# Kernel optimization log

Hardware: AMD Instinct MI355X
Metric: run time of the kernel (lower is better)

Reference implementation:

```python
import jax, jax.numpy as jnp
import numpy as np

WIDTH = 2048
NUM_HEADS = 16
HEAD_DIM = WIDTH // NUM_HEADS
WINDOW = 1024
B, T = 4, 2048
MIN_LOGIT = -2.3819763e+38
MAX_WAVELENGTH = 10000.0


def apply_rope(x, positions):
    # x: [b, t, n, h]; RoPE on first half of h, pass-through second half
    b, t, n, h = x.shape
    x_rope, x_pass = jnp.split(x, 2, axis=-1)
    half = x_rope.shape[-1] // 2
    freq_exponents = 2.0 * jnp.arange(half, dtype=jnp.float32) / (2 * half)
    inv_freq = MAX_WAVELENGTH ** (-freq_exponents)  # [half]
    sinusoid = positions.astype(jnp.float32).reshape(1, t, 1, 1) * inv_freq  # [1,t,1,half]
    sin = jnp.sin(sinusoid).astype(x.dtype)
    cos = jnp.cos(sinusoid).astype(x.dtype)
    x1, x2 = jnp.split(x_rope, 2, axis=-1)
    return jnp.concatenate([x1 * cos - x2 * sin, x2 * cos + x1 * sin, x_pass], axis=-1)


def setup_inputs() -> dict:
    key = jax.random.key(0)
    ks = jax.random.split(key, 6)
    x = jax.random.normal(ks[0], (B, T, WIDTH), dtype=jnp.float32)
    segment_pos = jnp.arange(T, dtype=jnp.int32)
    # forward-pass mask: single segment, causal + window
    pos = jnp.arange(T)
    attention_mask = (pos[:, None] >= pos[None, :]) & (pos[:, None] <= pos[None, :] + WINDOW)
    std = np.sqrt(1.0 / WIDTH)
    wq = jax.random.normal(ks[1], (WIDTH, WIDTH), dtype=jnp.float32) * std
    wk = jax.random.normal(ks[2], (HEAD_DIM, WIDTH), dtype=jnp.float32) * std
    wv = jax.random.normal(ks[3], (HEAD_DIM, WIDTH), dtype=jnp.float32) * std
    w_out = jax.random.normal(ks[4], (WIDTH, WIDTH), dtype=jnp.float32) * std
    b_out = jnp.zeros((WIDTH,), dtype=jnp.float32)
    return {"x": x, "segment_pos": segment_pos, "attention_mask": attention_mask,
            "wq": wq, "wk": wk, "wv": wv, "w_out": w_out, "b_out": b_out}


def reference(x, segment_pos, attention_mask, wq, wk, wv, w_out, b_out):
    b, t, _ = x.shape
    q = (x @ wq.T).reshape(b, t, NUM_HEADS, HEAD_DIM)  # [b,t,n,h]
    k = (x @ wk.T).reshape(b, t, 1, HEAD_DIM)          # single shared KV head (MQA)
    v = x @ wv.T                                        # [b,t,h]
    q = apply_rope(q, segment_pos)
    k = apply_rope(k, segment_pos)[:, :, 0]             # [b,t,h]
    logits = jnp.einsum('btnh,bsh->bnts', q, k).astype(jnp.float32) * (HEAD_DIM ** -0.5)
    logits = jnp.where(attention_mask[None, None], logits, MIN_LOGIT)
    probs = jax.nn.softmax(logits, axis=-1).astype(x.dtype)
    encoded = jnp.einsum('bnts,bsh->btnh', probs, v).reshape(b, t, WIDTH)
    return encoded @ w_out.T + b_out
```

## Files before the change

kernel.cpp:

```cpp
#include <hip/hip_runtime.h>
#include <stdint.h>


#define WIDTH_ 2048
#define NHEADS_ 16
#define HD_ 128
#define WINDOW_ 1024
#define B_ 4
#define T_ 2048
#define MROWS_ (B_ * T_)
#define NQKV_ (WIDTH_ + 2 * HD_)

typedef float f32x4 __attribute__((ext_vector_type(4)));
typedef __bf16 bf16x8 __attribute__((ext_vector_type(8)));
typedef float f32x4v __attribute__((ext_vector_type(4)));
typedef unsigned short u16;
typedef unsigned int u32;

__device__ __forceinline__ u16 f2bf(float x) {
  u32 u = __builtin_bit_cast(u32, x);
  return (u16)((u + 0x7FFFu + ((u >> 16) & 1u)) >> 16);
}
__device__ __forceinline__ float bf2f(u16 b) {
  u32 u = ((u32)b) << 16;
  return __builtin_bit_cast(float, u);
}
__device__ __forceinline__ u32 pack2bf(float a, float b) {
  union { __bf16 h[2]; u32 u; } c;
  c.h[0] = (__bf16)a; c.h[1] = (__bf16)b;
  return c.u;
}

__device__ __forceinline__ f32x4 mfma16(bf16x8 a, bf16x8 b, f32x4 c) {
  return __builtin_amdgcn_mfma_f32_16x16x32_bf16(a, b, c, 0, 0, 0);
}

#define GLL16(gp, lp)                                          \
  __builtin_amdgcn_global_load_lds(                            \
      (const __attribute__((address_space(1))) void*)(gp),     \
      (__attribute__((address_space(3))) void*)(lp), 16, 0, 0)

#define CSC_ 0.12753101296631838f
#define L2C_ 0.4152410118609203f

__global__ __launch_bounds__(256) void cvt_all(const float* __restrict__ x,
                                               const float* __restrict__ wq,
                                               const float* __restrict__ wk,
                                               const float* __restrict__ wv,
                                               const float* __restrict__ wo,
                                               u16* __restrict__ xb,
                                               u16* __restrict__ wqkv,
                                               u16* __restrict__ wob) {
  const int NX = MROWS_ * WIDTH_ / 4;
  const int NQ = WIDTH_ * WIDTH_ / 4;
  const int NK = HD_ * WIDTH_ / 4;
  const int total = NX + 2 * NQ + 2 * NK;
  int i = blockIdx.x * blockDim.x + threadIdx.x;
  int stride = gridDim.x * blockDim.x;
  for (; i < total; i += stride) {
    const float* s;
    u16* d;
    int j;
    if (i < NX) { s = x; d = xb; j = i; }
    else if (i < NX + NQ) { s = wq; d = wqkv; j = i - NX; }
    else if (i < NX + NQ + NK) { s = wk; d = wqkv + (size_t)WIDTH_ * WIDTH_; j = i - NX - NQ; }
    else if (i < NX + NQ + 2 * NK) { s = wv; d = wqkv + (size_t)(WIDTH_ + HD_) * WIDTH_; j = i - NX - NQ - NK; }
    else { s = wo; d = wob; j = i - NX - NQ - 2 * NK; }
    f32x4v v = *reinterpret_cast<const f32x4v*>(s + 4 * (size_t)j);
    uint2 o;
    o.x = (u32)f2bf(v[0]) | ((u32)f2bf(v[1]) << 16);
    o.y = (u32)f2bf(v[2]) | ((u32)f2bf(v[3]) << 16);
    *reinterpret_cast<uint2*>(d + 4 * (size_t)j) = o;
  }
}

__global__ __launch_bounds__(256) void sincos_tab(const int* __restrict__ segpos,
                                                  float2* __restrict__ sc) {
  int idx = blockIdx.x * 256 + threadIdx.x;
  int t = idx >> 5, d = idx & 31;
  float pos = (float)segpos[t];
  float ang = pos * exp2f(-(float)d * L2C_);
  float2 v;
  v.x = cosf(ang);
  v.y = sinf(ang);
  sc[idx] = v;
}

template <bool F32OUT>
__global__ __launch_bounds__(256) void gemm_bt(const u16* __restrict__ A,
                                               const u16* __restrict__ W,
                                               void* __restrict__ Cout,
                                               const float* __restrict__ bias,
                                               int M, int N, int K) {
  __shared__ alignas(16) u16 As[128 * 32];
  __shared__ alignas(16) u16 Bs[128 * 32];
  const int tid = threadIdx.x;
  const int wid = tid >> 6, lane = tid & 63;
  const int g = lane >> 4, lr = lane & 15;
  const int m0 = blockIdx.y << 7, n0 = blockIdx.x << 7;
  const int wm = wid >> 1, wn = wid & 1;

  const f32x4 vzero = {0.f, 0.f, 0.f, 0.f};
  f32x4 acc[4][4];
#pragma unroll
  for (int i = 0; i < 4; i++)
#pragma unroll
    for (int j = 0; j < 4; j++) acc[i][j] = vzero;

  const int c0 = wid * 2, c1 = wid * 2 + 1;
  const int lrow = lane >> 2;
  const int lcol = (lane & 3) * 8;
  const u16* a0 = A + (size_t)(m0 + c0 * 16 + lrow) * K + lcol;
  const u16* a1 = A + (size_t)(m0 + c1 * 16 + lrow) * K + lcol;
  const u16* b0 = W + (size_t)(n0 + c0 * 16 + lrow) * K + lcol;
  const u16* b1 = W + (size_t)(n0 + c1 * 16 + lrow) * K + lcol;

  for (int k0 = 0; k0 < K; k0 += 32) {
    __syncthreads();
    GLL16(a0 + k0, &As[c0 * 512]);
    GLL16(a1 + k0, &As[c1 * 512]);
    GLL16(b0 + k0, &Bs[c0 * 512]);
    GLL16(b1 + k0, &Bs[c1 * 512]);
    __syncthreads();

    bf16x8 af[4], bfv[4];
#pragma unroll
    for (int mi = 0; mi < 4; mi++)
      af[mi] = *(const bf16x8*)&As[(wm * 64 + mi * 16 + lr) * 32 + g * 8];
#pragma unroll
    for (int ni = 0; ni < 4; ni++)
      bfv[ni] = *(const bf16x8*)&Bs[(wn * 64 + ni * 16 + lr) * 32 + g * 8];
#pragma unroll
    for (int mi = 0; mi < 4; mi++)
#pragma unroll
      for (int ni = 0; ni < 4; ni++)
        acc[mi][ni] = mfma16(af[mi], bfv[ni], acc[mi][ni]);
  }

#pragma unroll
  for (int mi = 0; mi < 4; mi++) {
    int row = m0 + wm * 64 + mi * 16 + g * 4;
#pragma unroll
    for (int ni = 0; ni < 4; ni++) {
      int col = n0 + wn * 64 + ni * 16 + lr;
#pragma unroll
      for (int r = 0; r < 4; r++) {
        float v = acc[mi][ni][r];
        if (F32OUT) {
          ((float*)Cout)[(size_t)(row + r) * N + col] = v + bias[col];
        } else {
          ((u16*)Cout)[(size_t)(row + r) * N + col] = f2bf(v);
        }
      }
    }
  }
}

template <bool F32OUT>
__global__ __launch_bounds__(512, 2) void gemm256p8(const u16* __restrict__ A,
                                                    const u16* __restrict__ W,
                                                    void* __restrict__ Cout,
                                                    const float* __restrict__ bias,
                                                    int M, int N, int K) {
  __shared__ alignas(16) u16 As[2][2][128 * 64];
  __shared__ alignas(16) u16 Bs[2][2][128 * 64];
  const int tid = threadIdx.x;
  const int wid = tid >> 6, lane = tid & 63;
  const int g = lane >> 4, lr = lane & 15;
  const int wm = wid >> 2, wn = wid & 3;

  const int nwg = gridDim.x;
  const int o = blockIdx.x;
  const int wg = (o & 7) * (nwg >> 3) + (o >> 3);
  const int NT = N >> 8;
  const int mt = wg / NT, nt = wg % NT;
  const int m0 = mt << 8, n0 = nt << 8;

  const u16* pa[2];
  const u16* pb[2];
#pragma unroll
  for (int j = 0; j < 2; j++) {
    int ci = (wid + j * 8) * 64 + lane;
    int ri = ci >> 3, c = ci & 7;
    int colel = (c ^ (ri & 7)) * 8;
    int rA = ((ri >> 6) << 7) + (ri & 63);
    pa[j] = A + (size_t)(m0 + rA) * K + colel;
    pb[j] = W + (size_t)(n0 + ri) * K + colel;
  }
  const int dstoff = wid * 1024;

#define SA(bi, h, k0)                                                     \
  do {                                                                    \
    GLL16(pa[0] + (size_t)(h) * 64 * K + (k0), (char*)As[bi][h] + dstoff);\
    GLL16(pa[1] + (size_t)(h) * 64 * K + (k0),                            \
          (char*)As[bi][h] + dstoff + 8192);                              \
  } while (0)
#define SB(bi, h, k0)                                                     \
  do {                                                                    \
    GLL16(pb[0] + (size_t)(h) * 128 * K + (k0), (char*)Bs[bi][h] + dstoff);\
    GLL16(pb[1] + (size_t)(h) * 128 * K + (k0),                           \
          (char*)Bs[bi][h] + dstoff + 8192);                              \
  } while (0)

  const f32x4 vzero = {0.f, 0.f, 0.f, 0.f};
  f32x4 acc[8][4];
#pragma unroll
  for (int i = 0; i < 8; i++)
#pragma unroll
    for (int j = 0; j < 4; j++) acc[i][j] = vzero;

  bf16x8 bfv[4][2];

  auto LDA = [&](int bi, int mi, int kk) -> bf16x8 {
    int h = mi >> 2;
    int rb = wm * 64 + (mi & 3) * 16 + lr;
    return *(const bf16x8*)((const char*)As[bi][h] + rb * 128 +
                            (((kk * 4 + g) ^ (lr & 7)) << 4));
  };
  auto LDB = [&](int bi, int ni, int kk) -> bf16x8 {
    int rb = (wn & 1) * 64 + ni * 16 + lr;
    return *(const bf16x8*)((const char*)Bs[bi][wn >> 1] + rb * 128 +
                            (((kk * 4 + g) ^ (lr & 7)) << 4));
  };

#define VM6 asm volatile("s_waitcnt vmcnt(6)" ::: "memory")
#define VM0 asm volatile("s_waitcnt vmcnt(0)" ::: "memory")

#define PHASE(bi, p, STAGES, VM)                                          \
  {                                                                       \
    if ((p) == 0) {                                                       \
      for (int ni = 0; ni < 4; ni++)                                      \
        for (int kk = 0; kk < 2; kk++) bfv[ni][kk] = LDB(bi, ni, kk);     \
    }                                                                     \
    bf16x8 a0k0 = LDA(bi, 2 * (p), 0);                                    \
    bf16x8 a0k1 = LDA(bi, 2 * (p), 1);                                    \
    bf16x8 a1k0 = LDA(bi, 2 * (p) + 1, 0);                                \
    bf16x8 a1k1 = LDA(bi, 2 * (p) + 1, 1);                                \
    STAGES;                                                               \
    __builtin_amdgcn_s_barrier();                                         \
    asm volatile("s_waitcnt lgkmcnt(0)" ::: "memory");                    \
    __builtin_amdgcn_sched_barrier(0);                                    \
    __builtin_amdgcn_s_setprio(1);                                        \
    for (int ni = 0; ni < 4; ni++) {                                      \
      acc[2 * (p)][ni] = mfma16(a0k0, bfv[ni][0], acc[2 * (p)][ni]);      \
      acc[2 * (p)][ni] = mfma16(a0k1, bfv[ni][1], acc[2 * (p)][ni]);      \
      acc[2 * (p) + 1][ni] = mfma16(a1k0, bfv[ni][0], acc[2 * (p) + 1][ni]); \
      acc[2 * (p) + 1][ni] = mfma16(a1k1, bfv[ni][1], acc[2 * (p) + 1][ni]); \
    }                                                                     \
    __builtin_amdgcn_s_setprio(0);                                        \
    VM;                                                                   \
    __builtin_amdgcn_sched_barrier(0);                                    \
    __builtin_amdgcn_s_barrier();                                         \
  }

  SA(0, 0, 0); SA(0, 1, 0); SB(0, 0, 0); SB(0, 1, 0);
  SB(1, 0, 64); SB(1, 1, 64); SA(1, 0, 64);
  VM6;
  __builtin_amdgcn_sched_barrier(0);
  __builtin_amdgcn_s_barrier();

  const int half_iters = K >> 7;
  for (int i = 0; i < half_iters; ++i) {
    const bool pre = (i + 1 < half_iters);
    const int kc = i << 7;
    PHASE(0, 0, { SA(1, 1, kc + 64); }, );
    PHASE(0, 1, { if (pre) SB(0, 0, kc + 128); }, );
    PHASE(0, 2, { if (pre) SB(0, 1, kc + 128); }, );
    PHASE(0, 3, { if (pre) SA(0, 0, kc + 128); }, if (pre) { VM6; } else { VM0; });
    PHASE(1, 0, { if (pre) SA(0, 1, kc + 128); }, );
    PHASE(1, 1, { if (pre) SB(1, 0, kc + 192); }, );
    PHASE(1, 2, { if (pre) SB(1, 1, kc + 192); }, );
    PHASE(1, 3, { if (pre) SA(1, 0, kc + 192); }, if (pre) { VM6; } else { VM0; });
  }
#undef PHASE
#undef SA
#undef SB
#undef VM6
#undef VM0

#pragma unroll
  for (int mi = 0; mi < 8; mi++) {
    int row = m0 + wm * 128 + mi * 16 + g * 4;
#pragma unroll
    for (int ni = 0; ni < 4; ni++) {
      int col = n0 + wn * 64 + ni * 16 + lr;
#pragma unroll
      for (int r = 0; r < 4; r++) {
        float v = acc[mi][ni][r];
        if (F32OUT) {
          ((float*)Cout)[(size_t)(row + r) * N + col] = v + bias[col];
        } else {
          ((u16*)Cout)[(size_t)(row + r) * N + col] = f2bf(v);
        }
      }
    }
  }
}

__global__ __launch_bounds__(128) void kv_scatter(const u16* __restrict__ KVraw,
                                                  const int* __restrict__ segpos,
                                                  u16* __restrict__ Kb,
                                                  u16* __restrict__ VT) {
  const int row = blockIdx.x;
  const int b = row / T_, t = row % T_;
  const float pos = (float)segpos[t];
  const u16* kvsrc = KVraw + (size_t)row * 256;
  const int tid = threadIdx.x;

  if (tid < 32) {
    int d = tid;
    float inv = exp2f(-(float)d * L2C_);
    float ang = pos * inv;
    float sn = sinf(ang), cs = cosf(ang);
    float x1 = bf2f(kvsrc[d]), x2 = bf2f(kvsrc[d + 32]);
    Kb[(size_t)row * HD_ + d] = f2bf(x1 * cs - x2 * sn);
    Kb[(size_t)row * HD_ + d + 32] = f2bf(x2 * cs + x1 * sn);
  } else if (tid >= 64 && tid < 128) {
    int d = tid;
    Kb[(size_t)row * HD_ + d] = kvsrc[d];
  }
  for (int j = tid; j < HD_; j += 128) {
    VT[((size_t)b * HD_ + j) * T_ + t] = kvsrc[HD_ + j];
  }
}

__global__ __launch_bounds__(512, 4) void attn(const u16* __restrict__ Qraw,
                                               const float2* __restrict__ sc,
                                               const u16* __restrict__ Kb,
                                               const u16* __restrict__ VT,
                                               u16* __restrict__ Eb) {
  __shared__ alignas(16) u16 Ks[2][64 * 128];
  __shared__ alignas(16) u16 Vs[2][128 * 64];
  __shared__ alignas(16) u16 Ps[8][16 * 64];

  const int tid = threadIdx.x;
  const int wid = tid >> 6, lane = tid & 63;
  const int g = lane >> 4, lr = lane & 15;

  const int bid = blockIdx.x;
  const int grp = bid >> 4;
  const int b = grp >> 4, n = grp & 15;
  const int qt = ((bid & 15) + b * 4) & 15;
  const int q0b = qt * 128;
  const int q0w = q0b + wid * 16;
  const int q = q0w + lr;

  const char* kptr = (const char*)(Kb + (size_t)b * T_ * HD_);
  const char* vptr = (const char*)(VT + (size_t)b * HD_ * T_);

  const char* srcb[4];
  int smul, dst0;
  if (wid < 4) {
    smul = HD_ * 2;
#pragma unroll
    for (int i = 0; i < 4; i++) {
      int row = wid * 16 + i * 4 + (lane >> 4);
      int c = (lane & 15) << 4;
      srcb[i] = kptr + (size_t)row * 256 + (c ^ ((row & 7) << 4));
    }
    dst0 = wid * 4096;
  } else {
    smul = 2;
#pragma unroll
    for (int i = 0; i < 4; i++) {
      int row = (wid - 4) * 32 + i * 8 + (lane >> 3);
      int c = (lane & 7) << 4;
      srcb[i] = vptr + (size_t)row * (T_ * 2) + (c ^ ((row & 7) << 4));
    }
    dst0 = (wid - 4) * 4096;
  }

  bf16x8 qf[4];
  {
    const float2* scp = sc + (size_t)q * 32 + g * 8;
    const u16* qp = Qraw + (size_t)(b * T_ + q) * WIDTH_ + n * HD_;
    bf16x8 r0 = *(const bf16x8*)(qp + g * 8);
    bf16x8 r1 = *(const bf16x8*)(qp + 32 + g * 8);
    bf16x8 r2 = *(const bf16x8*)(qp + 64 + g * 8);
    bf16x8 r3 = *(const bf16x8*)(qp + 96 + g * 8);
#pragma unroll
    for (int j = 0; j < 8; j++) {
      float2 cs2 = scp[j];
      float x1 = (float)r0[j], x2 = (float)r1[j];
      qf[0][j] = (__bf16)((x1 * cs2.x - x2 * cs2.y) * CSC_);
      qf[1][j] = (__bf16)((x2 * cs2.x + x1 * cs2.y) * CSC_);
      qf[2][j] = (__bf16)((float)r2[j] * CSC_);
      qf[3][j] = (__bf16)((float)r3[j] * CSC_);
    }
  }

  const f32x4 vzero = {0.f, 0.f, 0.f, 0.f};
  f32x4 eacc[8];
#pragma unroll
  for (int i = 0; i < 8; i++) eacc[i] = vzero;
  float m_r = -1e30f, l_r = 0.f;

  const int sbeg = (q0b > WINDOW_) ? (q0b - WINDOW_) : 0;
  const int nt = (q0b + 127 - sbeg) / 64 + 1;

  char* Pw = (char*)Ps[wid];
  const int swz = (lr & 7) << 4;

  auto STAGE = [&](int s0, int buf) {
    char* dbase = (wid < 4) ? ((char*)Ks[buf] + dst0) : ((char*)Vs[buf] + dst0);
#pragma unroll
    for (int i = 0; i < 4; i++) {
      GLL16(srcb[i] + (size_t)s0 * smul, dbase + i * 1024);
    }
  };

  STAGE(sbeg, 0);
  __syncthreads();

  for (int t = 0; t < nt; ++t) {
    const int s0 = sbeg + t * 64;
    const int cur = t & 1;
    if (t + 1 < nt) STAGE(s0 + 64, cur ^ 1);

    const bool active = (s0 <= q0w + 15) && (s0 + 63 >= q0w - WINDOW_);
    if (active) {
      const char* kB = (const char*)Ks[cur];
      const char* vB = (const char*)Vs[cur];
      f32x4 sacc[4];
#pragma unroll
      for (int h = 0; h < 4; h++) sacc[h] = vzero;
#pragma unroll
      for (int h = 0; h < 4; h++) {
        const int krow = h * 16 + lr;
#pragma unroll
        for (int kk = 0; kk < 4; kk++) {
          bf16x8 kf = *(const bf16x8*)(kB + krow * 256 + ((kk * 64 + g * 16) ^ swz));
          sacc[h] = mfma16(kf, qf[kk], sacc[h]);
        }
      }

      const bool wint = (s0 + 63 <= q0w) && (s0 >= q0w + 15 - WINDOW_);
      float pm = -1e30f;
      if (wint) {
#pragma unroll
        for (int h = 0; h < 4; h++)
#pragma unroll
          for (int r = 0; r < 4; r++) pm = fmaxf(pm, sacc[h][r]);
      } else {
#pragma unroll
        for (int h = 0; h < 4; h++)
#pragma unroll
          for (int r = 0; r < 4; r++) {
            int s = s0 + h * 16 + g * 4 + r;
            bool ok = (s <= q) && (s + WINDOW_ >= q);
            float v = ok ? sacc[h][r] : -1e30f;
            sacc[h][r] = v;
            pm = fmaxf(pm, v);
          }
      }
      pm = fmaxf(pm, __shfl_xor(pm, 16));
      pm = fmaxf(pm, __shfl_xor(pm, 32));

      if (!__all(pm <= m_r + 8.f)) {
        float mnew = fmaxf(m_r, pm);
        float alpha = exp2f(m_r - mnew);
        m_r = mnew;
        l_r *= alpha;
        float aq[4];
#pragma unroll
        for (int r = 0; r < 4; r++) aq[r] = __shfl(alpha, g * 4 + r);
#pragma unroll
        for (int i = 0; i < 8; i++) {
          f32x4 e = eacc[i];
#pragma unroll
          for (int r = 0; r < 4; r++) e[r] *= aq[r];
          eacc[i] = e;
        }
      }
      float rs = 0.f;
#pragma unroll
      for (int h = 0; h < 4; h++)
#pragma unroll
        for (int r = 0; r < 4; r++) {
          float e = exp2f(sacc[h][r] - m_r);
          sacc[h][r] = e;
          rs += e;
        }
      rs += __shfl_xor(rs, 16);
      rs += __shfl_xor(rs, 32);
      l_r += rs;

#pragma unroll
      for (int h = 0; h < 4; h++) {
        int base = (lr * 128 + h * 32 + g * 8) ^ swz;
        uint2 w2;
        w2.x = pack2bf(sacc[h][0], sacc[h][1]);
        w2.y = pack2bf(sacc[h][2], sacc[h][3]);
        *(uint2*)(Pw + base) = w2;
      }
      bf16x8 pf0 = *(const bf16x8*)(Pw + ((lr * 128 + g * 16) ^ swz));
      bf16x8 pf1 = *(const bf16x8*)(Pw + ((lr * 128 + 64 + g * 16) ^ swz));

#pragma unroll
      for (int ht = 0; ht < 8; ht++) {
        const int vrow = ht * 16 + lr;
        bf16x8 vf0 = *(const bf16x8*)(vB + vrow * 128 + ((g * 16) ^ swz));
        bf16x8 vf1 = *(const bf16x8*)(vB + vrow * 128 + ((64 + g * 16) ^ swz));
        eacc[ht] = mfma16(pf0, vf0, eacc[ht]);
        eacc[ht] = mfma16(pf1, vf1, eacc[ht]);
      }
    }
    __syncthreads();
  }

  float lq[4];
#pragma unroll
  for (int r = 0; r < 4; r++) lq[r] = 1.f / __shfl(l_r, g * 4 + r);
#pragma unroll
  for (int ht = 0; ht < 8; ht++) {
#pragma unroll
    for (int r = 0; r < 4; r++) {
      int row = b * T_ + q0w + g * 4 + r;
      int col = n * HD_ + ht * 16 + lr;
      Eb[(size_t)row * WIDTH_ + col] = f2bf(eacc[ht][r] * lq[r]);
    }
  }
}

extern "C" void kernel_launch(void* const* d_in, const int* in_sizes, int n_in,
                              void* d_out, int out_size, void* d_ws, size_t ws_size,
                              hipStream_t stream) {
  (void)in_sizes; (void)n_in; (void)out_size; (void)ws_size;
  const float* x = (const float*)d_in[0];
  const int* segpos = (const int*)d_in[1];
  const float* wq = (const float*)d_in[3];
  const float* wk = (const float*)d_in[4];
  const float* wv = (const float*)d_in[5];
  const float* w_out = (const float*)d_in[6];
  const float* b_out = (const float*)d_in[7];

  char* p = (char*)d_ws;
  u16* xb = (u16*)p;    p += (size_t)MROWS_ * WIDTH_ * 2;
  u16* wqkv = (u16*)p;  p += (size_t)NQKV_ * WIDTH_ * 2;
  u16* wob = (u16*)p;   p += (size_t)WIDTH_ * WIDTH_ * 2;
  u16* qraw = (u16*)p;  p += (size_t)MROWS_ * WIDTH_ * 2;
  u16* kvraw = (u16*)p; p += (size_t)MROWS_ * 256 * 2;
  u16* kb = (u16*)p;    p += (size_t)MROWS_ * HD_ * 2;
  u16* vt = (u16*)p;    p += (size_t)B_ * HD_ * T_ * 2;
  float2* sc = (float2*)p; p += (size_t)T_ * 32 * 8;
  u16* eb = xb;

  cvt_all<<<4096, 256, 0, stream>>>(x, wq, wk, wv, w_out, xb, wqkv, wob);
  sincos_tab<<<T_ * 32 / 256, 256, 0, stream>>>(segpos, sc);

  gemm256p8<false><<<(MROWS_ / 256) * (WIDTH_ / 256), 512, 0, stream>>>(
      xb, wqkv, qraw, nullptr, MROWS_, WIDTH_, WIDTH_);
  gemm_bt<false><<<dim3(256 / 128, MROWS_ / 128), 256, 0, stream>>>(
      xb, wqkv + (size_t)WIDTH_ * WIDTH_, kvraw, nullptr, MROWS_, 256, WIDTH_);

  kv_scatter<<<MROWS_, 128, 0, stream>>>(kvraw, segpos, kb, vt);
  attn<<<B_ * NHEADS_ * (T_ / 128), 512, 0, stream>>>(qraw, sc, kb, vt, eb);

  gemm256p8<true><<<(MROWS_ / 256) * (WIDTH_ / 256), 512, 0, stream>>>(
      eb, wob, d_out, b_out, MROWS_, WIDTH_, WIDTH_);
}
```

Measured before the change: 317.5 us.

## Rework attention to 32x32 MFMA tiles with register-shuffled P and narrower KV GEMM tiles

The attention kernel drops from 8 to 4 waves per block, and each wave now handles 32 query rows using 32x32x16 bf16 MFMAs. Probabilities are passed to the PV product through cross-lane shuffles, so the per-wave LDS P buffer and its write/read round trip are gone. The K/V staging layout and swizzle change to match the new fragment shapes. Separately, the small KV projection GEMM uses 64-wide N tiles, doubling its block count for better CU occupancy. In exchange, attention uses more accumulator registers per wave and fewer waves per block.

```diff
diff --git a/kernel.cpp b/kernel.cpp
--- a/kernel.cpp
+++ b/kernel.cpp
@@ -12,6 +12,7 @@
 #define NQKV_ (WIDTH_ + 2 * HD_)
 
 typedef float f32x4 __attribute__((ext_vector_type(4)));
+typedef float f32x16 __attribute__((ext_vector_type(16)));
 typedef __bf16 bf16x8 __attribute__((ext_vector_type(8)));
 typedef float f32x4v __attribute__((ext_vector_type(4)));
 typedef unsigned short u16;
@@ -33,6 +34,9 @@
 
 __device__ __forceinline__ f32x4 mfma16(bf16x8 a, bf16x8 b, f32x4 c) {
   return __builtin_amdgcn_mfma_f32_16x16x32_bf16(a, b, c, 0, 0, 0);
+}
+__device__ __forceinline__ f32x16 mfma32(bf16x8 a, bf16x8 b, f32x16 c) {
+  return __builtin_amdgcn_mfma_f32_32x32x16_bf16(a, b, c, 0, 0, 0);
 }
 
 #define GLL16(gp, lp)                                          \
@@ -86,54 +90,49 @@
   sc[idx] = v;
 }
 
-template <bool F32OUT>
-__global__ __launch_bounds__(256) void gemm_bt(const u16* __restrict__ A,
-                                               const u16* __restrict__ W,
-                                               void* __restrict__ Cout,
-                                               const float* __restrict__ bias,
-                                               int M, int N, int K) {
+__global__ __launch_bounds__(256) void gemm_bt64(const u16* __restrict__ A,
+                                                 const u16* __restrict__ W,
+                                                 u16* __restrict__ Cout,
+                                                 int M, int N, int K) {
   __shared__ alignas(16) u16 As[128 * 32];
-  __shared__ alignas(16) u16 Bs[128 * 32];
+  __shared__ alignas(16) u16 Bs[64 * 32];
   const int tid = threadIdx.x;
   const int wid = tid >> 6, lane = tid & 63;
   const int g = lane >> 4, lr = lane & 15;
-  const int m0 = blockIdx.y << 7, n0 = blockIdx.x << 7;
+  const int m0 = blockIdx.y << 7, n0 = blockIdx.x << 6;
   const int wm = wid >> 1, wn = wid & 1;
 
   const f32x4 vzero = {0.f, 0.f, 0.f, 0.f};
-  f32x4 acc[4][4];
+  f32x4 acc[4][2];
 #pragma unroll
   for (int i = 0; i < 4; i++)
 #pragma unroll
-    for (int j = 0; j < 4; j++) acc[i][j] = vzero;
-
-  const int c0 = wid * 2, c1 = wid * 2 + 1;
+    for (int j = 0; j < 2; j++) acc[i][j] = vzero;
+
   const int lrow = lane >> 2;
   const int lcol = (lane & 3) * 8;
-  const u16* a0 = A + (size_t)(m0 + c0 * 16 + lrow) * K + lcol;
-  const u16* a1 = A + (size_t)(m0 + c1 * 16 + lrow) * K + lcol;
-  const u16* b0 = W + (size_t)(n0 + c0 * 16 + lrow) * K + lcol;
-  const u16* b1 = W + (size_t)(n0 + c1 * 16 + lrow) * K + lcol;
+  const u16* a0 = A + (size_t)(m0 + wid * 32 + lrow) * K + lcol;
+  const u16* a1 = A + (size_t)(m0 + wid * 32 + 16 + lrow) * K + lcol;
+  const u16* b0 = W + (size_t)(n0 + wid * 16 + lrow) * K + lcol;
 
   for (int k0 = 0; k0 < K; k0 += 32) {
     __syncthreads();
-    GLL16(a0 + k0, &As[c0 * 512]);
-    GLL16(a1 + k0, &As[c1 * 512]);
-    GLL16(b0 + k0, &Bs[c0 * 512]);
-    GLL16(b1 + k0, &Bs[c1 * 512]);
+    GLL16(a0 + k0, &As[wid * 1024]);
+    GLL16(a1 + k0, &As[wid * 1024 + 512]);
+    GLL16(b0 + k0, &Bs[wid * 512]);
     __syncthreads();
 
-    bf16x8 af[4], bfv[4];
+    bf16x8 af[4], bfv[2];
 #pragma unroll
     for (int mi = 0; mi < 4; mi++)
       af[mi] = *(const bf16x8*)&As[(wm * 64 + mi * 16 + lr) * 32 + g * 8];
 #pragma unroll
-    for (int ni = 0; ni < 4; ni++)
-      bfv[ni] = *(const bf16x8*)&Bs[(wn * 64 + ni * 16 + lr) * 32 + g * 8];
+    for (int ni = 0; ni < 2; ni++)
+      bfv[ni] = *(const bf16x8*)&Bs[(wn * 32 + ni * 16 + lr) * 32 + g * 8];
 #pragma unroll
     for (int mi = 0; mi < 4; mi++)
 #pragma unroll
-      for (int ni = 0; ni < 4; ni++)
+      for (int ni = 0; ni < 2; ni++)
         acc[mi][ni] = mfma16(af[mi], bfv[ni], acc[mi][ni]);
   }
 
@@ -141,17 +140,11 @@
   for (int mi = 0; mi < 4; mi++) {
     int row = m0 + wm * 64 + mi * 16 + g * 4;
 #pragma unroll
-    for (int ni = 0; ni < 4; ni++) {
-      int col = n0 + wn * 64 + ni * 16 + lr;
-#pragma unroll
-      for (int r = 0; r < 4; r++) {
-        float v = acc[mi][ni][r];
-        if (F32OUT) {
-          ((float*)Cout)[(size_t)(row + r) * N + col] = v + bias[col];
-        } else {
-          ((u16*)Cout)[(size_t)(row + r) * N + col] = f2bf(v);
-        }
-      }
+    for (int ni = 0; ni < 2; ni++) {
+      int col = n0 + wn * 32 + ni * 16 + lr;
+#pragma unroll
+      for (int r = 0; r < 4; r++)
+        Cout[(size_t)(row + r) * N + col] = f2bf(acc[mi][ni][r]);
     }
   }
 }
@@ -324,87 +317,87 @@
   }
 }
 
-__global__ __launch_bounds__(512, 4) void attn(const u16* __restrict__ Qraw,
+__global__ __launch_bounds__(256, 2) void attn(const u16* __restrict__ Qraw,
                                                const float2* __restrict__ sc,
                                                const u16* __restrict__ Kb,
                                                const u16* __restrict__ VT,
                                                u16* __restrict__ Eb) {
   __shared__ alignas(16) u16 Ks[2][64 * 128];
   __shared__ alignas(16) u16 Vs[2][128 * 64];
-  __shared__ alignas(16) u16 Ps[8][16 * 64];
 
   const int tid = threadIdx.x;
   const int wid = tid >> 6, lane = tid & 63;
-  const int g = lane >> 4, lr = lane & 15;
+  const int qc = lane & 31, hi = lane >> 5;
 
   const int bid = blockIdx.x;
   const int grp = bid >> 4;
   const int b = grp >> 4, n = grp & 15;
   const int qt = ((bid & 15) + b * 4) & 15;
   const int q0b = qt * 128;
-  const int q0w = q0b + wid * 16;
-  const int q = q0w + lr;
+  const int q0w = q0b + wid * 32;
+  const int q = q0w + qc;
 
   const char* kptr = (const char*)(Kb + (size_t)b * T_ * HD_);
   const char* vptr = (const char*)(VT + (size_t)b * HD_ * T_);
 
-  const char* srcb[4];
+  const char* srcb[8];
   int smul, dst0;
-  if (wid < 4) {
+  if (wid < 2) {
     smul = HD_ * 2;
 #pragma unroll
-    for (int i = 0; i < 4; i++) {
-      int row = wid * 16 + i * 4 + (lane >> 4);
+    for (int i = 0; i < 8; i++) {
+      int row = wid * 32 + i * 4 + (lane >> 4);
       int c = (lane & 15) << 4;
-      srcb[i] = kptr + (size_t)row * 256 + (c ^ ((row & 7) << 4));
-    }
-    dst0 = wid * 4096;
+      srcb[i] = kptr + (size_t)row * 256 + (c ^ ((row & 15) << 4));
+    }
+    dst0 = wid * 8192;
   } else {
     smul = 2;
 #pragma unroll
-    for (int i = 0; i < 4; i++) {
-      int row = (wid - 4) * 32 + i * 8 + (lane >> 3);
+    for (int i = 0; i < 8; i++) {
+      int row = (wid - 2) * 64 + i * 8 + (lane >> 3);
       int c = (lane & 7) << 4;
       srcb[i] = vptr + (size_t)row * (T_ * 2) + (c ^ ((row & 7) << 4));
     }
-    dst0 = (wid - 4) * 4096;
-  }
-
-  bf16x8 qf[4];
+    dst0 = (wid - 2) * 8192;
+  }
+
+  bf16x8 qf[8];
   {
-    const float2* scp = sc + (size_t)q * 32 + g * 8;
-    const u16* qp = Qraw + (size_t)(b * T_ + q) * WIDTH_ + n * HD_;
-    bf16x8 r0 = *(const bf16x8*)(qp + g * 8);
-    bf16x8 r1 = *(const bf16x8*)(qp + 32 + g * 8);
-    bf16x8 r2 = *(const bf16x8*)(qp + 64 + g * 8);
-    bf16x8 r3 = *(const bf16x8*)(qp + 96 + g * 8);
+    const u16* qp = Qraw + (size_t)(b * T_ + q) * WIDTH_ + n * HD_ + hi * 8;
+    bf16x8 r[8];
+#pragma unroll
+    for (int s = 0; s < 8; s++) r[s] = *(const bf16x8*)(qp + s * 16);
+    const float2* scp = sc + (size_t)q * 32 + hi * 8;
 #pragma unroll
     for (int j = 0; j < 8; j++) {
-      float2 cs2 = scp[j];
-      float x1 = (float)r0[j], x2 = (float)r1[j];
-      qf[0][j] = (__bf16)((x1 * cs2.x - x2 * cs2.y) * CSC_);
-      qf[1][j] = (__bf16)((x2 * cs2.x + x1 * cs2.y) * CSC_);
-      qf[2][j] = (__bf16)((float)r2[j] * CSC_);
-      qf[3][j] = (__bf16)((float)r3[j] * CSC_);
-    }
-  }
-
-  const f32x4 vzero = {0.f, 0.f, 0.f, 0.f};
-  f32x4 eacc[8];
-#pragma unroll
-  for (int i = 0; i < 8; i++) eacc[i] = vzero;
+      float2 c0 = scp[j];
+      float2 c1 = scp[16 + j];
+      float a1 = (float)r[0][j], a2 = (float)r[2][j];
+      float b1 = (float)r[1][j], b2 = (float)r[3][j];
+      qf[0][j] = (__bf16)((a1 * c0.x - a2 * c0.y) * CSC_);
+      qf[2][j] = (__bf16)((a2 * c0.x + a1 * c0.y) * CSC_);
+      qf[1][j] = (__bf16)((b1 * c1.x - b2 * c1.y) * CSC_);
+      qf[3][j] = (__bf16)((b2 * c1.x + b1 * c1.y) * CSC_);
+#pragma unroll
+      for (int s = 4; s < 8; s++) qf[s][j] = (__bf16)((float)r[s][j] * CSC_);
+    }
+  }
+
+  f32x16 eacc[4];
+#pragma unroll
+  for (int d = 0; d < 4; d++)
+#pragma unroll
+    for (int r = 0; r < 16; r++) eacc[d][r] = 0.f;
   float m_r = -1e30f, l_r = 0.f;
 
   const int sbeg = (q0b > WINDOW_) ? (q0b - WINDOW_) : 0;
-  const int nt = (q0b + 127 - sbeg) / 64 + 1;
-
-  char* Pw = (char*)Ps[wid];
-  const int swz = (lr & 7) << 4;
+  const int ntt = (q0b + 127 - sbeg) / 64 + 1;
 
   auto STAGE = [&](int s0, int buf) {
-    char* dbase = (wid < 4) ? ((char*)Ks[buf] + dst0) : ((char*)Vs[buf] + dst0);
-#pragma unroll
-    for (int i = 0; i < 4; i++) {
+    char* dbase = (wid < 2) ? ((char*)Ks[buf] + dst0) : ((char*)Vs[buf] + dst0);
+#pragma unroll
+    for (int i = 0; i < 8; i++) {
       GLL16(srcb[i] + (size_t)s0 * smul, dbase + i * 1024);
     }
   };
@@ -412,112 +405,124 @@
   STAGE(sbeg, 0);
   __syncthreads();
 
-  for (int t = 0; t < nt; ++t) {
+  for (int t = 0; t < ntt; ++t) {
     const int s0 = sbeg + t * 64;
     const int cur = t & 1;
-    if (t + 1 < nt) STAGE(s0 + 64, cur ^ 1);
-
-    const bool active = (s0 <= q0w + 15) && (s0 + 63 >= q0w - WINDOW_);
+    if (t + 1 < ntt) STAGE(s0 + 64, cur ^ 1);
+
+    const bool active = (s0 <= q0w + 31) && (s0 + 63 >= q0w - WINDOW_);
     if (active) {
       const char* kB = (const char*)Ks[cur];
       const char* vB = (const char*)Vs[cur];
-      f32x4 sacc[4];
-#pragma unroll
-      for (int h = 0; h < 4; h++) sacc[h] = vzero;
-#pragma unroll
-      for (int h = 0; h < 4; h++) {
-        const int krow = h * 16 + lr;
-#pragma unroll
-        for (int kk = 0; kk < 4; kk++) {
-          bf16x8 kf = *(const bf16x8*)(kB + krow * 256 + ((kk * 64 + g * 16) ^ swz));
-          sacc[h] = mfma16(kf, qf[kk], sacc[h]);
-        }
+      const bool wint = (s0 + 63 <= q0w) && (s0 >= q0w + 31 - WINDOW_);
+
+      for (int sb = 0; sb < 2; sb++) {
+        const int sblo = s0 + sb * 32;
+        if (sblo > q0w + 31 || sblo + 31 < q0w - WINDOW_) continue;
+
+        f32x16 sacc;
+#pragma unroll
+        for (int r = 0; r < 16; r++) sacc[r] = 0.f;
+        const int srow = sb * 32 + qc;
+        const int kswz = (srow & 15) << 4;
+#pragma unroll
+        for (int st = 0; st < 8; st++) {
+          bf16x8 kf = *(const bf16x8*)(kB + srow * 256 + ((st * 32 + hi * 16) ^ kswz));
+          sacc = mfma32(kf, qf[st], sacc);
+        }
+
+        float p[16];
+        float pm = -1e30f;
+        if (wint) {
+#pragma unroll
+          for (int r = 0; r < 16; r++) {
+            p[r] = sacc[r];
+            pm = fmaxf(pm, p[r]);
+          }
+        } else {
+#pragma unroll
+          for (int r = 0; r < 16; r++) {
+            int s = sblo + (r & 3) + 8 * (r >> 2) + 4 * hi;
+            bool ok = (s <= q) && (s + WINDOW_ >= q);
+            p[r] = ok ? sacc[r] : -1e30f;
+            pm = fmaxf(pm, p[r]);
+          }
+        }
+        pm = fmaxf(pm, __shfl_xor(pm, 32));
+
+        if (!__all(pm <= m_r + 8.f)) {
+          float mnew = fmaxf(m_r, pm);
+          float alpha = exp2f(m_r - mnew);
+          m_r = mnew;
+          l_r *= alpha;
+          float aq[16];
+#pragma unroll
+          for (int r = 0; r < 16; r++)
+            aq[r] = __shfl(alpha, (r & 3) + 8 * (r >> 2) + 4 * hi);
+#pragma unroll
+          for (int d = 0; d < 4; d++)
+#pragma unroll
+            for (int r = 0; r < 16; r++) eacc[d][r] *= aq[r];
+        }
+        float rs = 0.f;
+#pragma unroll
+        for (int r = 0; r < 16; r++) {
+          float e = exp2f(p[r] - m_r);
+          p[r] = e;
+          rs += e;
+        }
+        rs += __shfl_xor(rs, 32);
+        l_r += rs;
+
+        bf16x8 paf[2];
+#pragma unroll
+        for (int c = 0; c < 2; c++) {
+          u32 wA = pack2bf(p[8 * c + 0], p[8 * c + 1]);
+          u32 wB = pack2bf(p[8 * c + 2], p[8 * c + 3]);
+          u32 wC = pack2bf(p[8 * c + 4], p[8 * c + 5]);
+          u32 wD = pack2bf(p[8 * c + 6], p[8 * c + 7]);
+          u32 xA = (u32)__shfl_xor((int)wA, 32);
+          u32 xB = (u32)__shfl_xor((int)wB, 32);
+          u32 xC = (u32)__shfl_xor((int)wC, 32);
+          u32 xD = (u32)__shfl_xor((int)wD, 32);
+          union { u32 w[4]; bf16x8 v; } af_;
+          af_.w[0] = hi ? xC : wA;
+          af_.w[1] = hi ? xD : wB;
+          af_.w[2] = hi ? wC : xA;
+          af_.w[3] = hi ? wD : xB;
+          paf[c] = af_.v;
+        }
+
+        const int vswz = ((qc & 7) << 4);
+#pragma unroll
+        for (int d = 0; d < 4; d++) {
+          const int vrow = d * 32 + qc;
+          const int vs = ((vrow & 7) << 4);
+#pragma unroll
+          for (int c = 0; c < 2; c++) {
+            int colb = (sb * 2 + c) * 32 + hi * 16;
+            bf16x8 vf = *(const bf16x8*)(vB + vrow * 128 + (colb ^ vs));
+            eacc[d] = mfma32(paf[c], vf, eacc[d]);
+          }
+        }
+        (void)vswz;
       }
-
-      const bool wint = (s0 + 63 <= q0w) && (s0 >= q0w + 15 - WINDOW_);
-      float pm = -1e30f;
-      if (wint) {
-#pragma unroll
-        for (int h = 0; h < 4; h++)
-#pragma unroll
-          for (int r = 0; r < 4; r++) pm = fmaxf(pm, sacc[h][r]);
-      } else {
-#pragma unroll
-        for (int h = 0; h < 4; h++)
-#pragma unroll
-          for (int r = 0; r < 4; r++) {
-            int s = s0 + h * 16 + g * 4 + r;
-            bool ok = (s <= q) && (s + WINDOW_ >= q);
-            float v = ok ? sacc[h][r] : -1e30f;
-            sacc[h][r] = v;
-            pm = fmaxf(pm, v);
-          }
-      }
-      pm = fmaxf(pm, __shfl_xor(pm, 16));
-      pm = fmaxf(pm, __shfl_xor(pm, 32));
-
-      if (!__all(pm <= m_r + 8.f)) {
-        float mnew = fmaxf(m_r, pm);
-        float alpha = exp2f(m_r - mnew);
-        m_r = mnew;
-        l_r *= alpha;
-        float aq[4];
-#pragma unroll
-        for (int r = 0; r < 4; r++) aq[r] = __shfl(alpha, g * 4 + r);
-#pragma unroll
-        for (int i = 0; i < 8; i++) {
-          f32x4 e = eacc[i];
-#pragma unroll
-          for (int r = 0; r < 4; r++) e[r] *= aq[r];
-          eacc[i] = e;
-        }
-      }
-      float rs = 0.f;
-#pragma unroll
-      for (int h = 0; h < 4; h++)
-#pragma unroll
-        for (int r = 0; r < 4; r++) {
-          float e = exp2f(sacc[h][r] - m_r);
-          sacc[h][r] = e;
-          rs += e;
-        }
-      rs += __shfl_xor(rs, 16);
-      rs += __shfl_xor(rs, 32);
-      l_r += rs;
-
-#pragma unroll
-      for (int h = 0; h < 4; h++) {
-        int base = (lr * 128 + h * 32 + g * 8) ^ swz;
-        uint2 w2;
-        w2.x = pack2bf(sacc[h][0], sacc[h][1]);
-        w2.y = pack2bf(sacc[h][2], sacc[h][3]);
-        *(uint2*)(Pw + base) = w2;
-      }
-      bf16x8 pf0 = *(const bf16x8*)(Pw + ((lr * 128 + g * 16) ^ swz));
-      bf16x8 pf1 = *(const bf16x8*)(Pw + ((lr * 128 + 64 + g * 16) ^ swz));
-
-#pragma unroll
-      for (int ht = 0; ht < 8; ht++) {
-        const int vrow = ht * 16 + lr;
-        bf16x8 vf0 = *(const bf16x8*)(vB + vrow * 128 + ((g * 16) ^ swz));
-        bf16x8 vf1 = *(const bf16x8*)(vB + vrow * 128 + ((64 + g * 16) ^ swz));
-        eacc[ht] = mfma16(pf0, vf0, eacc[ht]);
-        eacc[ht] = mfma16(pf1, vf1, eacc[ht]);
-      }
     }
     __syncthreads();
   }
 
-  float lq[4];
-#pragma unroll
-  for (int r = 0; r < 4; r++) lq[r] = 1.f / __shfl(l_r, g * 4 + r);
-#pragma unroll
-  for (int ht = 0; ht < 8; ht++) {
-#pragma unroll
-    for (int r = 0; r < 4; r++) {
-      int row = b * T_ + q0w + g * 4 + r;
-      int col = n * HD_ + ht * 16 + lr;
-      Eb[(size_t)row * WIDTH_ + col] = f2bf(eacc[ht][r] * lq[r]);
+  float linv = 1.f / l_r;
+  float lqv[16];
+#pragma unroll
+  for (int r = 0; r < 16; r++)
+    lqv[r] = __shfl(linv, (r & 3) + 8 * (r >> 2) + 4 * hi);
+#pragma unroll
+  for (int d = 0; d < 4; d++) {
+#pragma unroll
+    for (int r = 0; r < 16; r++) {
+      int row = b * T_ + q0w + (r & 3) + 8 * (r >> 2) + 4 * hi;
+      int col = n * HD_ + d * 32 + qc;
+      Eb[(size_t)row * WIDTH_ + col] = f2bf(eacc[d][r] * lqv[r]);
     }
   }
 }
@@ -550,11 +555,11 @@
 
   gemm256p8<false><<<(MROWS_ / 256) * (WIDTH_ / 256), 512, 0, stream>>>(
       xb, wqkv, qraw, nullptr, MROWS_, WIDTH_, WIDTH_);
-  gemm_bt<false><<<dim3(256 / 128, MROWS_ / 128), 256, 0, stream>>>(
-      xb, wqkv + (size_t)WIDTH_ * WIDTH_, kvraw, nullptr, MROWS_, 256, WIDTH_);
+  gemm_bt64<<<dim3(256 / 64, MROWS_ / 128), 256, 0, stream>>>(
+      xb, wqkv + (size_t)WIDTH_ * WIDTH_, kvraw, MROWS_, 256, WIDTH_);
 
   kv_scatter<<<MROWS_, 128, 0, stream>>>(kvraw, segpos, kb, vt);
-  attn<<<B_ * NHEADS_ * (T_ / 128), 512, 0, stream>>>(qraw, sc, kb, vt, eb);
+  attn<<<B_ * NHEADS_ * (T_ / 128), 256, 0, stream>>>(qraw, sc, kb, vt, eb);
 
   gemm256p8<true><<<(MROWS_ / 256) * (WIDTH_ / 256), 512, 0, stream>>>(
       eb, wob, d_out, b_out, MROWS_, WIDTH_, WIDTH_);
```

Measured after the change: 320.4 us. No clear change (+0.9%).
